# Kernel tuning notes

Measured on AMD Instinct MI355X. Metric: run time of the kernel, lower is better.

Reference implementation:

```python
import jax, jax.numpy as jnp
import numpy as np

# BoxCoder weights and clamp from the torch module
WX, WY, WW, WH = 10.0, 10.0, 5.0, 5.0
BBOX_CLIP = float(np.log(1000.0 / 16.0))
SCORE_THRESH = 0.05
NMS_THRESH = 0.5
DET_PER_IMG = 100
MIN_SIZE = 0.01
B, N, C = 4, 4096, 91
IMG_H, IMG_W = 800, 1216


def setup_inputs() -> dict:
    key = jax.random.key(0)
    k1, k2, k3, k4, k5, k6 = jax.random.split(key, 6)
    class_logits = jax.random.normal(k1, (B * N, C), dtype=jnp.float32) * 2.0
    box_regression = jax.random.normal(k2, (B * N, C * 4), dtype=jnp.float32) * 0.5
    # valid xyxy proposals inside the image
    x1 = jax.random.uniform(k3, (B, N)) * (0.7 * IMG_W)
    y1 = jax.random.uniform(k4, (B, N)) * (0.7 * IMG_H)
    bw = jax.random.uniform(k5, (B, N)) * (0.25 * IMG_W) + 4.0
    bh = jax.random.uniform(k6, (B, N)) * (0.25 * IMG_H) + 4.0
    proposals = jnp.stack([x1, y1, x1 + bw, y1 + bh], axis=-1)
    image_shapes = jnp.tile(jnp.array([[IMG_H, IMG_W]], dtype=jnp.int32), (B, 1))
    return {"class_logits": class_logits, "box_regression": box_regression,
            "proposals": proposals, "image_shapes": image_shapes}


def decode_boxes(deltas, proposals):
    # deltas [N, C, 4], proposals [N, 4] xyxy -> pred boxes [N, C, 4]
    w = proposals[:, 2] - proposals[:, 0]
    h = proposals[:, 3] - proposals[:, 1]
    cx = proposals[:, 0] + 0.5 * w
    cy = proposals[:, 1] + 0.5 * h
    dx = deltas[..., 0] / WX
    dy = deltas[..., 1] / WY
    dw = jnp.minimum(deltas[..., 2] / WW, BBOX_CLIP)
    dh = jnp.minimum(deltas[..., 3] / WH, BBOX_CLIP)
    pcx = dx * w[:, None] + cx[:, None]
    pcy = dy * h[:, None] + cy[:, None]
    pw = jnp.exp(dw) * w[:, None]
    ph = jnp.exp(dh) * h[:, None]
    return jnp.stack([pcx - 0.5 * pw, pcy - 0.5 * ph,
                      pcx + 0.5 * pw, pcy + 0.5 * ph], axis=-1)


def iou_one_many(box, boxes):
    # box [4] vs boxes [M, 4]
    lt = jnp.maximum(box[:2], boxes[:, :2])
    rb = jnp.minimum(box[2:], boxes[:, 2:])
    wh = jnp.clip(rb - lt, 0.0)
    inter = wh[:, 0] * wh[:, 1]
    a1 = (box[2] - box[0]) * (box[3] - box[1])
    a2 = (boxes[:, 2] - boxes[:, 0]) * (boxes[:, 3] - boxes[:, 1])
    return inter / (a1 + a2 - inter)


def nms_keep(off_boxes, live):
    # greedy NMS on class-offset boxes; selection is non-differentiable
    off_boxes = jax.lax.stop_gradient(off_boxes)
    live = jax.lax.stop_gradient(live)

    def body(lv, _):
        i = jnp.argmax(lv)
        s = lv[i]
        iou = iou_one_many(off_boxes[i], off_boxes)
        lv = jnp.where(iou > NMS_THRESH, -jnp.inf, lv)
        lv = lv.at[i].set(-jnp.inf)
        return lv, (i, jnp.isfinite(s))

    _, (keep, kvalid) = jax.lax.scan(body, live, None, length=DET_PER_IMG)
    return keep, kvalid  # [DET_PER_IMG] each


def postprocess_one(logits, deltas, proposals, hw):
    # logits [N, C], deltas [N, C*4], proposals [N, 4], hw [2] float (H, W)
    num_classes = logits.shape[-1]
    boxes = decode_boxes(deltas.reshape(-1, num_classes, 4), proposals)  # [N, C, 4]
    Hh, Ww = hw[0], hw[1]
    boxes = jnp.stack([jnp.clip(boxes[..., 0], 0.0, Ww),
                       jnp.clip(boxes[..., 1], 0.0, Hh),
                       jnp.clip(boxes[..., 2], 0.0, Ww),
                       jnp.clip(boxes[..., 3], 0.0, Hh)], axis=-1)
    scores = jax.nn.softmax(logits, axis=-1)
    labels = jnp.broadcast_to(jnp.arange(num_classes, dtype=jnp.int32), scores.shape)
    # drop background class 0, flatten per-class candidates -> M = N*(C-1)
    boxes = boxes[:, 1:].reshape(-1, 4)
    scores = scores[:, 1:].reshape(-1)
    labels = labels[:, 1:].reshape(-1)
    ws = boxes[:, 2] - boxes[:, 0]
    hs = boxes[:, 3] - boxes[:, 1]
    valid = (scores > SCORE_THRESH) & (ws >= MIN_SIZE) & (hs >= MIN_SIZE)
    # batched_nms: per-class coordinate offset so classes never overlap
    max_coord = jnp.max(boxes)
    off_boxes = boxes + (labels.astype(boxes.dtype) * (max_coord + 1.0))[:, None]
    live = jnp.where(valid, scores, -jnp.inf)
    keep, kvalid = nms_keep(off_boxes, live)
    out_boxes = jnp.where(kvalid[:, None], boxes[keep], 0.0)
    out_scores = jnp.where(kvalid, scores[keep], 0.0)
    out_labels = jnp.where(kvalid, labels[keep], -1)
    return out_boxes, out_scores, out_labels


def reference(class_logits, box_regression, proposals, image_shapes):
    b, n, _ = proposals.shape
    num_classes = class_logits.shape[-1]
    logits = class_logits.reshape(b, n, num_classes)
    deltas = box_regression.reshape(b, n, num_classes * 4)
    hw = image_shapes.astype(logits.dtype)
    boxes, scores, labels = jax.vmap(postprocess_one)(logits, deltas, proposals, hw)
    return boxes, scores, labels
```

## Files before the change

kernel.cpp:

```cpp
#include <hip/hip_runtime.h>
#include <math.h>
#include <float.h>
#include <limits.h>

#define NBATCH 4
#define NPROP  4096
#define NCLS   91
#define NFG    90
#define NDET   100
#define CCAP   1024
#define BN     (NBATCH * NPROP)
#define SLOTS  (NFG * NDET)
#define FCAP   16384
#define CHUNK  128
#define CPAD   32

static __device__ __forceinline__ float clampf(float x, float lo, float hi) {
    return fminf(fmaxf(x, lo), hi);
}

static __device__ __forceinline__ void decode_box(int b, int np, int c,
    const float* __restrict__ props, const float* __restrict__ deltas,
    float W, float H, float& bx1, float& by1, float& bx2, float& by2)
{
    const float* pr = props + ((size_t)b * NPROP + np) * 4;
    const float x1 = pr[0], y1 = pr[1], x2 = pr[2], y2 = pr[3];
    const float w = x2 - x1, h = y2 - y1;
    const float cx = x1 + 0.5f * w, cy = y1 + 0.5f * h;
    const float* d = deltas + (((size_t)b * NPROP + np) * NCLS + c) * 4;
    const float BBC = 4.135166556742356f;
    const float dx = d[0] / 10.0f;
    const float dy = d[1] / 10.0f;
    const float dw = fminf(d[2] / 5.0f, BBC);
    const float dh = fminf(d[3] / 5.0f, BBC);
    const float pcx = dx * w + cx;
    const float pcy = dy * h + cy;
    const float pw = expf(dw) * w;
    const float ph = expf(dh) * h;
    bx1 = clampf(pcx - 0.5f * pw, 0.0f, W);
    by1 = clampf(pcy - 0.5f * ph, 0.0f, H);
    bx2 = clampf(pcx + 0.5f * pw, 0.0f, W);
    by2 = clampf(pcy + 0.5f * ph, 0.0f, H);
}

static __device__ __forceinline__ bool iou_gt(const float4 S, const float4 Q, float aq)
{
    const float iw = fmaxf(fminf(S.z, Q.z) - fmaxf(S.x, Q.x), 0.0f);
    const float ih = fmaxf(fminf(S.w, Q.w) - fmaxf(S.y, Q.y), 0.0f);
    const float inter = iw * ih;
    const float as = (S.z - S.x) * (S.w - S.y);
    return inter / (as + aq - inter) > 0.5f;
}

static __device__ __forceinline__ int block_excl_scan(int v, int t, int* wtot)
{
    const int lane = t & 63, wid = t >> 6;
    int inc = v;
    #pragma unroll
    for (int s = 1; s < 64; s <<= 1) {
        const int u = __shfl_up(inc, s);
        if (lane >= s) inc += u;
    }
    if (lane == 63) wtot[wid] = inc;
    __syncthreads();
    int base = 0;
    for (int w2 = 0; w2 < wid; ++w2) base += wtot[w2];
    __syncthreads();
    return base + inc - v;
}

__global__ __launch_bounds__(256) void zero_kernel(int* __restrict__ cntPad)
{
    const int i = blockIdx.x * 256 + threadIdx.x;
    if (i < NBATCH * NFG * CPAD) cntPad[i] = 0;
}

__global__ __launch_bounds__(256) void fused_decode_kernel(
    const float* __restrict__ logits, const float* __restrict__ props,
    const float* __restrict__ deltas, const int* __restrict__ imgsh,
    int* __restrict__ cntPad, unsigned long long* __restrict__ cKeys,
    float4* __restrict__ cBox)
{
    const int wavei = threadIdx.x >> 6;
    const int lane  = threadIdx.x & 63;
    const int p = blockIdx.x * 4 + wavei;
    const int b = p >> 12;
    const int np = p & (NPROP - 1);
    const float* lrow = logits + (size_t)p * NCLS;

    const float a  = lrow[lane];
    const float a2 = (lane + 64 < NCLS) ? lrow[lane + 64] : -INFINITY;

    float m = fmaxf(a, a2);
    #pragma unroll
    for (int s = 32; s > 0; s >>= 1) m = fmaxf(m, __shfl_down(m, s));
    m = __shfl(m, 0);

    const float e0 = expf(a - m);
    const float e1 = (lane + 64 < NCLS) ? expf(a2 - m) : 0.0f;
    float sum = e0 + e1;
    #pragma unroll
    for (int s = 32; s > 0; s >>= 1) sum += __shfl_down(sum, s);
    sum = __shfl(sum, 0);

    const float W = (float)imgsh[b * 2 + 1];
    const float H = (float)imgsh[b * 2 + 0];

    #pragma unroll
    for (int half = 0; half < 2; ++half) {
        const int c = lane + half * 64;
        if (c < 1 || c >= NCLS) continue;
        const float e = half ? e1 : e0;
        const float score = e / sum;
        if (!(score > 0.05f)) continue;
        float bx1, by1, bx2, by2;
        decode_box(b, np, c, props, deltas, W, H, bx1, by1, bx2, by2);
        if (!((bx2 - bx1) >= 0.01f && (by2 - by1) >= 0.01f)) continue;
        const int cm1 = c - 1;
        const unsigned flat = (unsigned)(np * NFG + cm1);
        const unsigned long long key =
            ((unsigned long long)__float_as_uint(score) << 32) | (unsigned)(~flat);
        const int bucket = b * NFG + cm1;
        const int pos = atomicAdd(&cntPad[bucket * CPAD], 1);
        if (pos < CCAP) {
            cKeys[(size_t)bucket * CCAP + pos] = key;
            cBox[(size_t)bucket * CCAP + pos]  = make_float4(bx1, by1, bx2, by2);
        }
    }
}

__global__ __launch_bounds__(256) void class_nms_kernel(
    const int* __restrict__ cntPad, const unsigned long long* __restrict__ cKeys,
    const float4* __restrict__ cBox, unsigned long long* __restrict__ svKeys)
{
    const int blk  = blockIdx.x;
    const int t    = threadIdx.x;

    __shared__ unsigned long long sk[CCAP];
    __shared__ unsigned long long sks[CCAP];
    __shared__ float4 sboxS[CCAP];
    __shared__ unsigned long long mrow[CHUNK][2];
    __shared__ float4 sOwn[NDET];
    __shared__ unsigned long long sPreW[2];
    __shared__ int s_ns;

    const int n = min(cntPad[blk * CPAD], CCAP);
    if (n == 0) {
        for (int i = t; i < NDET; i += 256) svKeys[(size_t)blk * NDET + i] = 0ULL;
        return;
    }
    const unsigned long long* srcK = cKeys + (size_t)blk * CCAP;
    const float4* srcB = cBox + (size_t)blk * CCAP;
    for (int i = t; i < n; i += 256) sk[i] = srcK[i];
    __syncthreads();

    {
        unsigned long long myk[4];
        float4 myb[4];
        int rnk[4] = {0, 0, 0, 0};
        #pragma unroll
        for (int e = 0; e < 4; ++e) {
            const int i = t + e * 256;
            myk[e] = (i < n) ? sk[i] : 0ULL;
            myb[e] = (i < n) ? srcB[i] : make_float4(0.f, 0.f, 0.f, 0.f);
        }
        #pragma unroll 4
        for (int j = 0; j < n; ++j) {
            const unsigned long long kj = sk[j];
            #pragma unroll
            for (int e = 0; e < 4; ++e) rnk[e] += (kj > myk[e]) ? 1 : 0;
        }
        #pragma unroll
        for (int e = 0; e < 4; ++e) {
            if (t + e * 256 < n) { sks[rnk[e]] = myk[e]; sboxS[rnk[e]] = myb[e]; }
        }
    }
    if (t == 0) s_ns = 0;
    __syncthreads();

    int nsTot = 0;
    for (int cb = 0; cb < n && nsTot < NDET; cb += CHUNK) {
        const int C = min(CHUNK, n - cb);

        bool pre = false;
        if (t < C) {
            const float4 Q = sboxS[cb + t];
            const float aq = (Q.z - Q.x) * (Q.w - Q.y);
            for (int l = 0; l < nsTot; ++l) {
                if (iou_gt(sOwn[l], Q, aq)) { pre = true; break; }
            }
        }
        const unsigned long long bal = __ballot(pre);
        if (t == 0)  sPreW[0] = bal;
        if (t == 64) sPreW[1] = bal;

        {
            const int r = t >> 1, w = t & 1;
            unsigned long long word = 0ULL;
            if (r < C) {
                const float4 R = sboxS[cb + r];
                const int j0 = w * 64;
                const int jend = min(j0 + 64, C);
                for (int j = (j0 > r + 1 ? j0 : r + 1); j < jend; ++j) {
                    const float4 Q = sboxS[cb + j];
                    const float aq = (Q.z - Q.x) * (Q.w - Q.y);
                    if (iou_gt(R, Q, aq)) word |= (1ULL << (j - j0));
                }
            }
            mrow[r][w] = word;
        }
        __syncthreads();

        if (t == 0) {
            unsigned long long S0 = sPreW[0], S1 = sPreW[1];
            int ns = nsTot;
            unsigned long long r0 = mrow[0][0], r1 = mrow[0][1];
            for (int i = 0; i < C && ns < NDET; ++i) {
                const unsigned long long nr0 = (i + 1 < C) ? mrow[i + 1][0] : 0ULL;
                const unsigned long long nr1 = (i + 1 < C) ? mrow[i + 1][1] : 0ULL;
                const bool dead = (i < 64) ? ((S0 >> i) & 1ULL)
                                           : ((S1 >> (i - 64)) & 1ULL);
                if (!dead) {
                    sOwn[ns] = sboxS[cb + i];
                    svKeys[(size_t)blk * NDET + ns] = sks[cb + i];
                    ++ns;
                    S0 |= r0; S1 |= r1;
                }
                r0 = nr0; r1 = nr1;
            }
            s_ns = ns;
        }
        __syncthreads();
        nsTot = s_ns;
    }

    for (int i = nsTot + t; i < NDET; i += 256) svKeys[(size_t)blk * NDET + i] = 0ULL;
}

__global__ __launch_bounds__(1024) void select_kernel(
    const unsigned long long* __restrict__ svKeys,
    const float* __restrict__ props, const float* __restrict__ deltas,
    const int* __restrict__ imgsh, float* __restrict__ out)
{
    const int b = blockIdx.x;
    const int t = threadIdx.x;
    __shared__ unsigned long long F[FCAP];
    __shared__ int hist[4096];
    __shared__ int wtot[16];
    __shared__ int s_T, s_above, s_total;

    if (t == 0) { s_T = -1; s_above = 0; s_total = 0; }
    #pragma unroll
    for (int j = 0; j < 4; ++j) hist[t + j * 1024] = 0;

    const unsigned long long* src = svKeys + (size_t)b * SLOTS;
    unsigned long long keys[9];
    #pragma unroll
    for (int j = 0; j < 9; ++j) {
        const int s = t + j * 1024;
        keys[j] = (s < SLOTS) ? src[s] : 0ULL;
    }
    __syncthreads();

    #pragma unroll
    for (int j = 0; j < 9; ++j) {
        if (keys[j] != 0ULL) atomicAdd(&hist[(unsigned)(keys[j] >> 52)], 1);
    }
    __syncthreads();

    {
        const int gbase = (1023 - t) * 4;
        const int s0 = hist[gbase] + hist[gbase + 1] + hist[gbase + 2] + hist[gbase + 3];
        const int pre = block_excl_scan(s0, t, wtot);
        int acc = pre;
        for (int d = gbase + 3; d >= gbase; --d) {
            const int h = hist[d];
            if (acc < NDET && acc + h >= NDET) { s_T = d; s_above = acc; }
            acc += h;
        }
        if (t == 1023) s_total = acc;
    }
    __syncthreads();

    const int T = s_T;
    const int total = s_total;
    const int n2 = (T < 0) ? total : (s_above + hist[T]);
    const bool fast = (n2 <= 2048);

    int mycnt = 0;
    #pragma unroll
    for (int j = 0; j < 9; ++j) {
        const unsigned long long k = keys[j];
        const bool m = (k != 0ULL) && (fast ? (T < 0 || (int)(k >> 52) >= T) : true);
        mycnt += m ? 1 : 0;
    }
    int off = block_excl_scan(mycnt, t, wtot);
    #pragma unroll
    for (int j = 0; j < 9; ++j) {
        const unsigned long long k = keys[j];
        const bool m = (k != 0ULL) && (fast ? (T < 0 || (int)(k >> 52) >= T) : true);
        if (m) F[off++] = k;
    }
    const int nsort = fast ? n2 : total;

    int P = 128; while (P < nsort) P <<= 1;
    for (int i = nsort + t; i < P; i += 1024) F[i] = 0ULL;

    for (unsigned kk = 2; kk <= (unsigned)P; kk <<= 1) {
        for (unsigned jj = kk >> 1; jj > 0; jj >>= 1) {
            __syncthreads();
            for (unsigned i = t; i < (unsigned)P; i += 1024) {
                const unsigned ixj = i ^ jj;
                if (ixj > i) {
                    const unsigned long long x = F[i], y = F[ixj];
                    const bool up = ((i & kk) == 0);
                    if (up ? (x < y) : (x > y)) { F[i] = y; F[ixj] = x; }
                }
            }
        }
    }
    __syncthreads();

    float* oB = out + (size_t)b * NDET * 4;
    float* oS = out + (size_t)NBATCH * NDET * 4 + (size_t)b * NDET;
    float* oL = out + (size_t)NBATCH * NDET * 5 + (size_t)b * NDET;
    if (t < NDET) {
        const unsigned long long key = F[t];
        if (key != 0ULL) {
            const unsigned flat = ~(unsigned)key;
            const float score = __uint_as_float((unsigned)(key >> 32));
            const int np = flat / NFG;
            const int c  = (int)(flat - (unsigned)np * NFG) + 1;
            const float W = (float)imgsh[b * 2 + 1];
            const float H = (float)imgsh[b * 2 + 0];
            float bx1, by1, bx2, by2;
            decode_box(b, np, c, props, deltas, W, H, bx1, by1, bx2, by2);
            oB[t * 4 + 0] = bx1; oB[t * 4 + 1] = by1;
            oB[t * 4 + 2] = bx2; oB[t * 4 + 3] = by2;
            oS[t] = score;
            oL[t] = (float)c;
        } else {
            oB[t * 4 + 0] = 0.0f; oB[t * 4 + 1] = 0.0f;
            oB[t * 4 + 2] = 0.0f; oB[t * 4 + 3] = 0.0f;
            oS[t] = 0.0f; oL[t] = -1.0f;
        }
    }
}

extern "C" void kernel_launch(void* const* d_in, const int* in_sizes, int n_in,
                              void* d_out, int out_size, void* d_ws, size_t ws_size,
                              hipStream_t stream)
{
    const float* logits = (const float*)d_in[0];
    const float* deltas = (const float*)d_in[1];
    const float* props  = (const float*)d_in[2];
    const int*   imgsh  = (const int*)d_in[3];
    float* out = (float*)d_out;

    char* w = (char*)d_ws;
    int* cntPad = (int*)w;                 w += (size_t)NBATCH * NFG * CPAD * sizeof(int);
    unsigned long long* svKeys = (unsigned long long*)w;
    w += (size_t)NBATCH * SLOTS * sizeof(unsigned long long);
    unsigned long long* cKeys = (unsigned long long*)w;
    w += (size_t)NBATCH * NFG * CCAP * sizeof(unsigned long long);
    float4* cBox = (float4*)w;
    w += (size_t)NBATCH * NFG * CCAP * sizeof(float4);

    const int nz = (NBATCH * NFG * CPAD + 255) / 256;
    zero_kernel<<<nz, 256, 0, stream>>>(cntPad);
    fused_decode_kernel<<<BN / 4, 256, 0, stream>>>(
        logits, props, deltas, imgsh, cntPad, cKeys, cBox);
    class_nms_kernel<<<NBATCH * NFG, 256, 0, stream>>>(cntPad, cKeys, cBox, svKeys);
    select_kernel<<<NBATCH, 1024, 0, stream>>>(svKeys, props, deltas, imgsh, out);
}
```

Baseline: 76.51 us.

## Fuse per-class NMS and top-k selection via last-block-done counter

```diff
diff --git a/kernel.cpp b/kernel.cpp
--- a/kernel.cpp
+++ b/kernel.cpp
@@ -11,9 +11,10 @@
 #define CCAP   1024
 #define BN     (NBATCH * NPROP)
 #define SLOTS  (NFG * NDET)
-#define FCAP   16384
 #define CHUNK  128
 #define CPAD   32
+
+typedef unsigned long long ull;
 
 static __device__ __forceinline__ float clampf(float x, float lo, float hi) {
     return fminf(fmaxf(x, lo), hi);
@@ -72,14 +73,13 @@
 __global__ __launch_bounds__(256) void zero_kernel(int* __restrict__ cntPad)
 {
     const int i = blockIdx.x * 256 + threadIdx.x;
-    if (i < NBATCH * NFG * CPAD) cntPad[i] = 0;
+    if (i < NBATCH * NFG * CPAD + 256) cntPad[i] = 0;
 }
 
 __global__ __launch_bounds__(256) void fused_decode_kernel(
     const float* __restrict__ logits, const float* __restrict__ props,
     const float* __restrict__ deltas, const int* __restrict__ imgsh,
-    int* __restrict__ cntPad, unsigned long long* __restrict__ cKeys,
-    float4* __restrict__ cBox)
+    int* __restrict__ cntPad, ull* __restrict__ cKeys, float4* __restrict__ cBox)
 {
     const int wavei = threadIdx.x >> 6;
     const int lane  = threadIdx.x & 63;
@@ -118,8 +118,7 @@
         if (!((bx2 - bx1) >= 0.01f && (by2 - by1) >= 0.01f)) continue;
         const int cm1 = c - 1;
         const unsigned flat = (unsigned)(np * NFG + cm1);
-        const unsigned long long key =
-            ((unsigned long long)__float_as_uint(score) << 32) | (unsigned)(~flat);
+        const ull key = ((ull)__float_as_uint(score) << 32) | (unsigned)(~flat);
         const int bucket = b * NFG + cm1;
         const int pos = atomicAdd(&cntPad[bucket * CPAD], 1);
         if (pos < CCAP) {
@@ -129,203 +128,224 @@
     }
 }
 
-__global__ __launch_bounds__(256) void class_nms_kernel(
-    const int* __restrict__ cntPad, const unsigned long long* __restrict__ cKeys,
-    const float4* __restrict__ cBox, unsigned long long* __restrict__ svKeys)
-{
-    const int blk  = blockIdx.x;
-    const int t    = threadIdx.x;
-
-    __shared__ unsigned long long sk[CCAP];
-    __shared__ unsigned long long sks[CCAP];
-    __shared__ float4 sboxS[CCAP];
-    __shared__ unsigned long long mrow[CHUNK][2];
-    __shared__ float4 sOwn[NDET];
-    __shared__ unsigned long long sPreW[2];
-    __shared__ int s_ns;
-
-    const int n = min(cntPad[blk * CPAD], CCAP);
-    if (n == 0) {
-        for (int i = t; i < NDET; i += 256) svKeys[(size_t)blk * NDET + i] = 0ULL;
-        return;
-    }
-    const unsigned long long* srcK = cKeys + (size_t)blk * CCAP;
-    const float4* srcB = cBox + (size_t)blk * CCAP;
-    for (int i = t; i < n; i += 256) sk[i] = srcK[i];
-    __syncthreads();
-
-    {
-        unsigned long long myk[4];
-        float4 myb[4];
-        int rnk[4] = {0, 0, 0, 0};
-        #pragma unroll
-        for (int e = 0; e < 4; ++e) {
-            const int i = t + e * 256;
-            myk[e] = (i < n) ? sk[i] : 0ULL;
-            myb[e] = (i < n) ? srcB[i] : make_float4(0.f, 0.f, 0.f, 0.f);
-        }
-        #pragma unroll 4
-        for (int j = 0; j < n; ++j) {
-            const unsigned long long kj = sk[j];
-            #pragma unroll
-            for (int e = 0; e < 4; ++e) rnk[e] += (kj > myk[e]) ? 1 : 0;
-        }
-        #pragma unroll
-        for (int e = 0; e < 4; ++e) {
-            if (t + e * 256 < n) { sks[rnk[e]] = myk[e]; sboxS[rnk[e]] = myb[e]; }
-        }
-    }
-    if (t == 0) s_ns = 0;
-    __syncthreads();
-
-    int nsTot = 0;
-    for (int cb = 0; cb < n && nsTot < NDET; cb += CHUNK) {
-        const int C = min(CHUNK, n - cb);
-
-        bool pre = false;
-        if (t < C) {
-            const float4 Q = sboxS[cb + t];
-            const float aq = (Q.z - Q.x) * (Q.w - Q.y);
-            for (int l = 0; l < nsTot; ++l) {
-                if (iou_gt(sOwn[l], Q, aq)) { pre = true; break; }
-            }
-        }
-        const unsigned long long bal = __ballot(pre);
-        if (t == 0)  sPreW[0] = bal;
-        if (t == 64) sPreW[1] = bal;
-
-        {
-            const int r = t >> 1, w = t & 1;
-            unsigned long long word = 0ULL;
-            if (r < C) {
-                const float4 R = sboxS[cb + r];
-                const int j0 = w * 64;
-                const int jend = min(j0 + 64, C);
-                for (int j = (j0 > r + 1 ? j0 : r + 1); j < jend; ++j) {
-                    const float4 Q = sboxS[cb + j];
-                    const float aq = (Q.z - Q.x) * (Q.w - Q.y);
-                    if (iou_gt(R, Q, aq)) word |= (1ULL << (j - j0));
-                }
-            }
-            mrow[r][w] = word;
-        }
-        __syncthreads();
-
-        if (t == 0) {
-            unsigned long long S0 = sPreW[0], S1 = sPreW[1];
-            int ns = nsTot;
-            unsigned long long r0 = mrow[0][0], r1 = mrow[0][1];
-            for (int i = 0; i < C && ns < NDET; ++i) {
-                const unsigned long long nr0 = (i + 1 < C) ? mrow[i + 1][0] : 0ULL;
-                const unsigned long long nr1 = (i + 1 < C) ? mrow[i + 1][1] : 0ULL;
-                const bool dead = (i < 64) ? ((S0 >> i) & 1ULL)
-                                           : ((S1 >> (i - 64)) & 1ULL);
-                if (!dead) {
-                    sOwn[ns] = sboxS[cb + i];
-                    svKeys[(size_t)blk * NDET + ns] = sks[cb + i];
-                    ++ns;
-                    S0 |= r0; S1 |= r1;
-                }
-                r0 = nr0; r1 = nr1;
-            }
-            s_ns = ns;
-        }
-        __syncthreads();
-        nsTot = s_ns;
-    }
-
-    for (int i = nsTot + t; i < NDET; i += 256) svKeys[(size_t)blk * NDET + i] = 0ULL;
-}
-
-__global__ __launch_bounds__(1024) void select_kernel(
-    const unsigned long long* __restrict__ svKeys,
+__global__ __launch_bounds__(256) void nms_select_kernel(
+    const int* __restrict__ cntPad, const ull* __restrict__ cKeys,
+    const float4* __restrict__ cBox, ull* __restrict__ svKeys,
+    int* __restrict__ done,
     const float* __restrict__ props, const float* __restrict__ deltas,
     const int* __restrict__ imgsh, float* __restrict__ out)
 {
-    const int b = blockIdx.x;
-    const int t = threadIdx.x;
-    __shared__ unsigned long long F[FCAP];
-    __shared__ int hist[4096];
-    __shared__ int wtot[16];
-    __shared__ int s_T, s_above, s_total;
-
-    if (t == 0) { s_T = -1; s_above = 0; s_total = 0; }
-    #pragma unroll
-    for (int j = 0; j < 4; ++j) hist[t + j * 1024] = 0;
-
-    const unsigned long long* src = svKeys + (size_t)b * SLOTS;
-    unsigned long long keys[9];
-    #pragma unroll
-    for (int j = 0; j < 9; ++j) {
-        const int s = t + j * 1024;
-        keys[j] = (s < SLOTS) ? src[s] : 0ULL;
-    }
-    __syncthreads();
-
-    #pragma unroll
-    for (int j = 0; j < 9; ++j) {
-        if (keys[j] != 0ULL) atomicAdd(&hist[(unsigned)(keys[j] >> 52)], 1);
-    }
-    __syncthreads();
+    const int blk  = blockIdx.x;
+    const int b    = blk / NFG;
+    const int t    = threadIdx.x;
+    const int lane = t & 63, wid = t >> 6;
+
+    __shared__ __align__(16) ull smem[4608];
+    __shared__ int s_ns, s_last, s_T, s_above, s_total, wtot[4];
+    __shared__ ull s_best;
 
     {
-        const int gbase = (1023 - t) * 4;
-        const int s0 = hist[gbase] + hist[gbase + 1] + hist[gbase + 2] + hist[gbase + 3];
+        ull* sk       = smem;
+        ull* sks      = smem + 1024;
+        float4* sboxS = (float4*)(smem + 2048);
+        ull (*mrow)[2] = (ull (*)[2])(smem + 4096);
+        float4* sOwn  = (float4*)(smem + 4352);
+        ull* sPreW    = smem + 4552;
+
+        const int n = min(cntPad[blk * CPAD], CCAP);
+        if (n == 0) {
+            for (int i = t; i < NDET; i += 256) svKeys[(size_t)blk * NDET + i] = 0ULL;
+        } else {
+            const ull* srcK = cKeys + (size_t)blk * CCAP;
+            const float4* srcB = cBox + (size_t)blk * CCAP;
+            for (int i = t; i < n; i += 256) sk[i] = srcK[i];
+            __syncthreads();
+
+            {
+                ull myk[4]; float4 myb[4]; int rnk[4] = {0, 0, 0, 0};
+                #pragma unroll
+                for (int e = 0; e < 4; ++e) {
+                    const int i = t + e * 256;
+                    myk[e] = (i < n) ? sk[i] : 0ULL;
+                    myb[e] = (i < n) ? srcB[i] : make_float4(0.f, 0.f, 0.f, 0.f);
+                }
+                #pragma unroll 4
+                for (int j = 0; j < n; ++j) {
+                    const ull kj = sk[j];
+                    #pragma unroll
+                    for (int e = 0; e < 4; ++e) rnk[e] += (kj > myk[e]) ? 1 : 0;
+                }
+                #pragma unroll
+                for (int e = 0; e < 4; ++e)
+                    if (t + e * 256 < n) { sks[rnk[e]] = myk[e]; sboxS[rnk[e]] = myb[e]; }
+            }
+            if (t == 0) s_ns = 0;
+            __syncthreads();
+
+            int nsTot = 0;
+            for (int cb = 0; cb < n && nsTot < NDET; cb += CHUNK) {
+                const int C = min(CHUNK, n - cb);
+                bool pre = false;
+                if (t < C) {
+                    const float4 Q = sboxS[cb + t];
+                    const float aq = (Q.z - Q.x) * (Q.w - Q.y);
+                    for (int l = 0; l < nsTot; ++l)
+                        if (iou_gt(sOwn[l], Q, aq)) { pre = true; break; }
+                }
+                const ull bal = __ballot(pre);
+                if (t == 0)  sPreW[0] = bal;
+                if (t == 64) sPreW[1] = bal;
+                {
+                    const int r = t >> 1, w = t & 1;
+                    ull word = 0ULL;
+                    if (r < C) {
+                        const float4 R = sboxS[cb + r];
+                        const int j0 = w * 64;
+                        const int jend = min(j0 + 64, C);
+                        for (int j = (j0 > r + 1 ? j0 : r + 1); j < jend; ++j) {
+                            const float4 Q = sboxS[cb + j];
+                            const float aq = (Q.z - Q.x) * (Q.w - Q.y);
+                            if (iou_gt(R, Q, aq)) word |= (1ULL << (j - j0));
+                        }
+                    }
+                    mrow[r][w] = word;
+                }
+                __syncthreads();
+                if (t == 0) {
+                    ull S0 = sPreW[0], S1 = sPreW[1];
+                    int ns = nsTot;
+                    ull r0 = mrow[0][0], r1 = mrow[0][1];
+                    for (int i = 0; i < C && ns < NDET; ++i) {
+                        const ull nr0 = (i + 1 < C) ? mrow[i + 1][0] : 0ULL;
+                        const ull nr1 = (i + 1 < C) ? mrow[i + 1][1] : 0ULL;
+                        const bool dead = (i < 64) ? ((S0 >> i) & 1ULL)
+                                                   : ((S1 >> (i - 64)) & 1ULL);
+                        if (!dead) {
+                            sOwn[ns] = sboxS[cb + i];
+                            svKeys[(size_t)blk * NDET + ns] = sks[cb + i];
+                            ++ns;
+                            S0 |= r0; S1 |= r1;
+                        }
+                        r0 = nr0; r1 = nr1;
+                    }
+                    s_ns = ns;
+                }
+                __syncthreads();
+                nsTot = s_ns;
+            }
+            for (int i = nsTot + t; i < NDET; i += 256) svKeys[(size_t)blk * NDET + i] = 0ULL;
+        }
+    }
+
+    __syncthreads();
+    __threadfence();
+    if (t == 0) {
+        s_last = (atomicAdd(&done[b], 1) == NFG - 1) ? 1 : 0;
+        s_T = -1; s_above = 0; s_total = 0;
+    }
+    __syncthreads();
+    if (!s_last) return;
+    __threadfence();
+
+    ull* F      = smem;
+    int* hist   = (int*)(smem + 2048);
+    ull* chosen = smem + 4096;
+    ull* wred   = smem + 4196;
+
+    for (int i = t; i < 4096; i += 256) hist[i] = 0;
+    for (int i = t; i < NDET; i += 256) chosen[i] = 0ULL;
+    __syncthreads();
+
+    const ull* src = svKeys + (size_t)b * SLOTS;
+    for (int s = t; s < SLOTS; s += 256) {
+        const ull k = src[s];
+        if (k) atomicAdd(&hist[(unsigned)(k >> 52)], 1);
+    }
+    __syncthreads();
+
+    {
+        const int gbase = (255 - t) * 16;
+        int s0 = 0;
+        #pragma unroll
+        for (int j = 0; j < 16; ++j) s0 += hist[gbase + j];
         const int pre = block_excl_scan(s0, t, wtot);
         int acc = pre;
-        for (int d = gbase + 3; d >= gbase; --d) {
+        for (int d = gbase + 15; d >= gbase; --d) {
             const int h = hist[d];
             if (acc < NDET && acc + h >= NDET) { s_T = d; s_above = acc; }
             acc += h;
         }
-        if (t == 1023) s_total = acc;
-    }
-    __syncthreads();
-
-    const int T = s_T;
-    const int total = s_total;
+        if (t == 255) s_total = acc;
+    }
+    __syncthreads();
+
+    const int T = s_T, total = s_total;
     const int n2 = (T < 0) ? total : (s_above + hist[T]);
-    const bool fast = (n2 <= 2048);
-
-    int mycnt = 0;
-    #pragma unroll
-    for (int j = 0; j < 9; ++j) {
-        const unsigned long long k = keys[j];
-        const bool m = (k != 0ULL) && (fast ? (T < 0 || (int)(k >> 52) >= T) : true);
-        mycnt += m ? 1 : 0;
-    }
-    int off = block_excl_scan(mycnt, t, wtot);
-    #pragma unroll
-    for (int j = 0; j < 9; ++j) {
-        const unsigned long long k = keys[j];
-        const bool m = (k != 0ULL) && (fast ? (T < 0 || (int)(k >> 52) >= T) : true);
-        if (m) F[off++] = k;
-    }
-    const int nsort = fast ? n2 : total;
-
-    int P = 128; while (P < nsort) P <<= 1;
-    for (int i = nsort + t; i < P; i += 1024) F[i] = 0ULL;
-
-    for (unsigned kk = 2; kk <= (unsigned)P; kk <<= 1) {
-        for (unsigned jj = kk >> 1; jj > 0; jj >>= 1) {
-            __syncthreads();
-            for (unsigned i = t; i < (unsigned)P; i += 1024) {
-                const unsigned ixj = i ^ jj;
-                if (ixj > i) {
-                    const unsigned long long x = F[i], y = F[ixj];
-                    const bool up = ((i & kk) == 0);
-                    if (up ? (x < y) : (x > y)) { F[i] = y; F[ixj] = x; }
-                }
-            }
-        }
-    }
-    __syncthreads();
+
+    if (n2 <= 2048) {
+        int mycnt = 0;
+        for (int s = t; s < SLOTS; s += 256) {
+            const ull k = src[s];
+            if (k && (T < 0 || (int)(k >> 52) >= T)) ++mycnt;
+        }
+        int off = block_excl_scan(mycnt, t, wtot);
+        for (int s = t; s < SLOTS; s += 256) {
+            const ull k = src[s];
+            if (k && (T < 0 || (int)(k >> 52) >= T)) F[off++] = k;
+        }
+        __syncthreads();
+        ull myk[8]; int rnk[8];
+        #pragma unroll
+        for (int e = 0; e < 8; ++e) {
+            const int i = t + e * 256;
+            myk[e] = (i < n2) ? F[i] : 0ULL;
+            rnk[e] = 0;
+        }
+        for (int j = 0; j < n2; ++j) {
+            const ull kj = F[j];
+            #pragma unroll
+            for (int e = 0; e < 8; ++e) rnk[e] += (kj > myk[e]) ? 1 : 0;
+        }
+        __syncthreads();
+        #pragma unroll
+        for (int e = 0; e < 8; ++e) {
+            const int i = t + e * 256;
+            if (i < n2 && rnk[e] < NDET) chosen[rnk[e]] = myk[e];
+        }
+        __syncthreads();
+    } else {
+        ull ub = ~0ULL;
+        for (int r = 0; r < NDET; ++r) {
+            ull best = 0ULL;
+            for (int s = t; s < SLOTS; s += 256) {
+                const ull k = src[s];
+                if (k < ub && k > best) best = k;
+            }
+            #pragma unroll
+            for (int o = 32; o > 0; o >>= 1) {
+                const ull ob = __shfl_down(best, o);
+                if (ob > best) best = ob;
+            }
+            if (lane == 0) wred[wid] = best;
+            __syncthreads();
+            if (t == 0) {
+                ull mx = wred[0];
+                for (int w2 = 1; w2 < 4; ++w2) if (wred[w2] > mx) mx = wred[w2];
+                s_best = mx;
+                if (mx) chosen[r] = mx;
+            }
+            __syncthreads();
+            if (s_best == 0ULL) break;
+            ub = s_best;
+            __syncthreads();
+        }
+    }
 
     float* oB = out + (size_t)b * NDET * 4;
     float* oS = out + (size_t)NBATCH * NDET * 4 + (size_t)b * NDET;
     float* oL = out + (size_t)NBATCH * NDET * 5 + (size_t)b * NDET;
     if (t < NDET) {
-        const unsigned long long key = F[t];
+        const ull key = chosen[t];
         if (key != 0ULL) {
             const unsigned flat = ~(unsigned)key;
             const float score = __uint_as_float((unsigned)(key >> 32));
@@ -358,18 +378,21 @@
     float* out = (float*)d_out;
 
     char* w = (char*)d_ws;
-    int* cntPad = (int*)w;                 w += (size_t)NBATCH * NFG * CPAD * sizeof(int);
-    unsigned long long* svKeys = (unsigned long long*)w;
-    w += (size_t)NBATCH * SLOTS * sizeof(unsigned long long);
-    unsigned long long* cKeys = (unsigned long long*)w;
-    w += (size_t)NBATCH * NFG * CCAP * sizeof(unsigned long long);
+    int* cntPad = (int*)w;
+    w += (size_t)(NBATCH * NFG * CPAD + 256) * sizeof(int);
+    ull* svKeys = (ull*)w;
+    w += (size_t)NBATCH * SLOTS * sizeof(ull);
+    ull* cKeys = (ull*)w;
+    w += (size_t)NBATCH * NFG * CCAP * sizeof(ull);
     float4* cBox = (float4*)w;
     w += (size_t)NBATCH * NFG * CCAP * sizeof(float4);
 
-    const int nz = (NBATCH * NFG * CPAD + 255) / 256;
+    int* done = cntPad + NBATCH * NFG * CPAD;
+
+    const int nz = (NBATCH * NFG * CPAD + 256 + 255) / 256;
     zero_kernel<<<nz, 256, 0, stream>>>(cntPad);
     fused_decode_kernel<<<BN / 4, 256, 0, stream>>>(
         logits, props, deltas, imgsh, cntPad, cKeys, cBox);
-    class_nms_kernel<<<NBATCH * NFG, 256, 0, stream>>>(cntPad, cKeys, cBox, svKeys);
-    select_kernel<<<NBATCH, 1024, 0, stream>>>(svKeys, props, deltas, imgsh, out);
-}
+    nms_select_kernel<<<NBATCH * NFG, 256, 0, stream>>>(
+        cntPad, cKeys, cBox, svKeys, done, props, deltas, imgsh, out);
+}
```

Result: slower. 114.7 us (+49.9%).
